# Optimization experiments

Measured on AMD Instinct MI355X. Metric: run time of the kernel, lower is better.

The kernel has to match this reference:

```python
import jax, jax.numpy as jnp
import numpy as np

N, C_IN, C_OUT, T, V = 64, 128, 128, 128, 25
REL = C_IN // 8  # rel_channels = 16


def setup_inputs() -> dict:
    key = jax.random.key(0)
    ks = jax.random.split(key, 12)
    s_in = 1.0 / np.sqrt(C_IN)
    s_rel = 1.0 / np.sqrt(REL)
    return {
        "x": jax.random.normal(ks[0], (N, C_IN, T, V), jnp.float32),
        "A": jax.random.normal(ks[1], (V, V), jnp.float32),
        "alpha": jnp.float32(1.0),
        "W1": jax.random.normal(ks[2], (REL, C_IN), jnp.float32) * s_in,
        "b1": jnp.zeros((REL,), jnp.float32),
        "W2": jax.random.normal(ks[3], (REL, C_IN), jnp.float32) * s_in,
        "b2": jnp.zeros((REL,), jnp.float32),
        "W3": jax.random.normal(ks[4], (C_OUT, C_IN), jnp.float32) * s_in,
        "b3": jnp.zeros((C_OUT,), jnp.float32),
        "W4": jax.random.normal(ks[5], (C_OUT, REL), jnp.float32) * s_rel,
        "b4": jnp.zeros((C_OUT,), jnp.float32),
    }


def reference(x, A, alpha, W1, b1, W2, b2, W3, b3, W4, b4):
    # conv1(x).mean(-2) and conv2(x).mean(-2): 1x1 conv is linear, so mean over
    # T commutes with it -> compute mean first to avoid an (N,REL,T,V) temp.
    xm = x.mean(axis=2)                                        # (N, C, V)
    x1 = jnp.einsum('rc,ncv->nrv', W1, xm) + b1[None, :, None]  # (N, R, V)
    x2 = jnp.einsum('rc,ncv->nrv', W2, xm) + b2[None, :, None]  # (N, R, V)
    x3 = jnp.einsum('oc,nctv->notv', W3, x) + b3[None, :, None, None]  # (N,O,T,V)
    # tanh of broadcasted pairwise difference: (N, R, V, V)
    d = jnp.tanh(x1[:, :, :, None] - x2[:, :, None, :])
    # conv4 (1x1 over channel dim) -> learned per-channel adjacency
    adj = jnp.einsum('or,nrvu->novu', W4, d) + b4[None, :, None, None]
    adj = adj * alpha + A[None, None, :, :]                    # (N, O, V, V)
    return jnp.einsum('ncvu,nctv->nctu', adj, x3)              # (N, O, T, V)
```

## Files before the change

### kernel.cpp

```cpp
#include <hip/hip_runtime.h>


#define NB   64
#define CIN  128
#define COUT 128
#define TT   128
#define VV   25
#define REL  16

#define JT 25
#define KT 4
#define XF_BYTES (JT * KT * 1024)
#define XH_BYTES 51200
#define X3_STRIDE 1040
#define LDS_BYTES (64 * X3_STRIDE)
#define TSTRIDE 416
#define XMP_PLANE (NB * CIN * VV)

typedef __attribute__((ext_vector_type(8))) short bf16x8;
typedef __attribute__((ext_vector_type(4))) float f32x4;

__device__ inline short f2bf(float f) {
    unsigned u = __float_as_uint(f);
    u += 0x7fff + ((u >> 16) & 1);
    return (short)(u >> 16);
}

__launch_bounds__(256)
__global__ void k_prep(const float* __restrict__ x, float* __restrict__ xmp,
                       char* __restrict__ Xf) {
    __shared__ float tile[32 * TSTRIDE];
    int tid = threadIdx.x;
    int kt = blockIdx.x >> 3, tb = blockIdx.x & 7, n = blockIdx.y;
    int c0 = kt * 32;

    const float* src = x + (size_t)(n * CIN + c0) * 3200 + tb * 400;
#pragma unroll
    for (int p = 0; p < 13; ++p) {
        int i = tid + p * 256;
        if (i < 3200) {
            int c = i / 100, q = i - c * 100;
            int sw = ((c >> 3) & 1) << 4;
            *reinterpret_cast<float4*>(&tile[c * TSTRIDE + ((q * 4) ^ sw)]) =
                *reinterpret_cast<const float4*>(src + (size_t)c * 3200 + q * 4);
        }
    }
    __syncthreads();

#pragma unroll
    for (int pp = 0; pp < 4; ++pp) {
        int p = tid + pp * 256;
        if (p < 800) {
            int c = p / 25, v = p - c * 25;
            int sw = ((c >> 3) & 1) << 4;
            float s = 0.f;
#pragma unroll
            for (int t = 0; t < 16; ++t) s += tile[c * TSTRIDE + ((t * 25 + v) ^ sw)];
            xmp[(size_t)tb * XMP_PLANE + ((size_t)n * CIN + c0 + c) * VV + v] = s;
        }
    }

    char* dst = Xf + (size_t)(n * 8 + tb) * XF_BYTES + (size_t)kt * 25600;
    for (int ch = tid; ch < 1600; ch += 256) {
        int l = ch & 63, jt = ch >> 6;
        int j = jt * 16 + (l & 15);
        int cl = 8 * (l >> 4);
        int sw = ((l >> 4) & 1) << 4;
        bf16x8 v;
#pragma unroll
        for (int b = 0; b < 8; ++b)
            v[b] = f2bf(tile[(cl + b) * TSTRIDE + (j ^ sw)]);
        *reinterpret_cast<bf16x8*>(dst + (size_t)ch * 16) = v;
    }
}

__global__ void k_adj(const float* __restrict__ xmp,
                      const float* __restrict__ A, const float* __restrict__ alphap,
                      const float* __restrict__ W1, const float* __restrict__ b1,
                      const float* __restrict__ W2, const float* __restrict__ b2,
                      const float* __restrict__ W4, const float* __restrict__ b4,
                      const float* __restrict__ W3, char* __restrict__ W3f,
                      char* __restrict__ adjT) {
    __shared__ char adjS[32 * 2048];
    __shared__ float xms[CIN * VV];
    __shared__ float W1s[REL * CIN];
    __shared__ float W2s[REL * CIN];
    __shared__ float x1s[REL * VV];
    __shared__ float x2s[REL * VV];
    __shared__ float W4s[32 * REL];
    __shared__ float b4s[32];

    int tid = threadIdx.x;
    int n = blockIdx.x;
    int o0 = blockIdx.y * 32;

    if (n == 0) {
#pragma unroll
        for (int pass = 0; pass < 2; ++pass) {
            int chunk = blockIdx.y * 512 + pass * 256 + tid;
            int l = chunk & 63;
            int frag = chunk >> 6;
            int ct = frag >> 2, kt = frag & 3;
            int c = ct * 16 + (l & 15);
            int kb = kt * 32 + 8 * (l >> 4);
            const float4 f0 = *reinterpret_cast<const float4*>(&W3[(size_t)c * CIN + kb]);
            const float4 f1 = *reinterpret_cast<const float4*>(&W3[(size_t)c * CIN + kb + 4]);
            bf16x8 vv;
            vv[0] = f2bf(f0.x); vv[1] = f2bf(f0.y); vv[2] = f2bf(f0.z); vv[3] = f2bf(f0.w);
            vv[4] = f2bf(f1.x); vv[5] = f2bf(f1.y); vv[6] = f2bf(f1.z); vv[7] = f2bf(f1.w);
            *reinterpret_cast<bf16x8*>(W3f + (size_t)chunk * 16) = vv;
        }
    }

    for (int i = tid; i < 16384; i += 256) reinterpret_cast<float*>(adjS)[i] = 0.f;
    for (int i = tid; i < CIN * VV; i += 256) {
        float s = 0.f;
#pragma unroll
        for (int tb = 0; tb < 8; ++tb)
            s += xmp[(size_t)tb * XMP_PLANE + (size_t)n * CIN * VV + i];
        xms[i] = s * (1.0f / TT);
    }
    for (int i = tid; i < REL * CIN; i += 256) { W1s[i] = W1[i]; W2s[i] = W2[i]; }
    for (int i = tid; i < 32 * REL; i += 256) W4s[i] = W4[o0 * REL + i];
    if (tid < 32) b4s[tid] = b4[o0 + tid];
    __syncthreads();

    for (int task = tid; task < 2 * REL * VV; task += 256) {
        int rv = task % (REL * VV);
        int which = task / (REL * VV);
        int r = rv / VV, v = rv % VV;
        const float* Ws = which ? W2s : W1s;
        float s = 0.f;
#pragma unroll 8
        for (int c = 0; c < CIN; ++c) s = fmaf(Ws[r * CIN + c], xms[c * VV + v], s);
        s += which ? b2[r] : b1[r];
        (which ? x2s : x1s)[rv] = s;
    }
    __syncthreads();

    float alpha = alphap[0];
    for (int p = tid; p < VV * VV; p += 256) {
        int v = p / VV, u = p % VV;
        float d[REL];
#pragma unroll
        for (int r = 0; r < REL; ++r) d[r] = tanhf(x1s[r * VV + v] - x2s[r * VV + u]);
        float Avu = A[v * VV + u];
        int off = (u >> 4) * 1024 + (((u & 15) + 16 * (v >> 3)) * 16) + (v & 7) * 2;
        for (int oo = 0; oo < 32; ++oo) {
            float s = 0.f;
#pragma unroll
            for (int r = 0; r < REL; ++r) s = fmaf(W4s[oo * REL + r], d[r], s);
            float val = alpha * (s + b4s[oo]) + Avu;
            *(short*)(adjS + oo * 2048 + off) = f2bf(val);
        }
    }
    __syncthreads();

    float4* dst = reinterpret_cast<float4*>(adjT + (size_t)(n * COUT + o0) * 2048);
    const float4* src = reinterpret_cast<const float4*>(adjS);
    for (int i = tid; i < 4096; i += 256) dst[i] = src[i];
}

__launch_bounds__(1024)
__global__ void k_main(const char* __restrict__ Xf, const char* __restrict__ W3f,
                       const float* __restrict__ b3, const char* __restrict__ adjT,
                       float* __restrict__ out) {
    __shared__ __align__(16) char lds[LDS_BYTES];

    int tid = threadIdx.x;
    int tb = blockIdx.x, n = blockIdx.y;
    int lane = tid & 63, w = tid >> 6;
    int g = lane >> 4, lr = lane & 15;
    int ct = w >> 1, jh = w & 1;
    int jt0 = jh ? 13 : 0;
    int njt = jh ? 12 : 13;

    const char* xfb = Xf + (size_t)(n * 8 + tb) * XF_BYTES;

    f32x4 acc[13];
#pragma unroll
    for (int u = 0; u < 13; ++u) acc[u] = f32x4{0.f, 0.f, 0.f, 0.f};

#pragma unroll
    for (int h = 0; h < 2; ++h) {
#pragma unroll
        for (int q = 0; q < 4; ++q) {
            int chunk = tid + q * 1024;
            if (chunk < 3200)
                *reinterpret_cast<bf16x8*>(lds + (size_t)chunk * 16) =
                    *reinterpret_cast<const bf16x8*>(
                        xfb + (size_t)h * XH_BYTES + (size_t)chunk * 16);
        }
        __syncthreads();
#pragma unroll
        for (int kk = 0; kk < 2; ++kk) {
            int kt = h * 2 + kk;
            bf16x8 a = *reinterpret_cast<const bf16x8*>(
                W3f + (size_t)((ct * 4 + kt) * 64 + lane) * 16);
#pragma unroll
            for (int u = 0; u < 13; ++u) {
                if (u < njt) {
                    int jt = jt0 + u;
                    bf16x8 bx = *reinterpret_cast<const bf16x8*>(
                        lds + (size_t)((kk * JT + jt) * 64 + lane) * 16);
                    acc[u] = __builtin_amdgcn_mfma_f32_16x16x32_bf16(a, bx, acc[u], 0, 0, 0);
                }
            }
        }
        __syncthreads();
    }

    float bv[4];
#pragma unroll
    for (int r = 0; r < 4; ++r) bv[r] = b3[ct * 16 + 4 * g + r];

    const char* adjTb = adjT + (size_t)(n * COUT) * 2048;
    int t0 = tb * 16;

#pragma unroll
    for (int hh = 0; hh < 2; ++hh) {
        if ((ct >> 2) == hh) {
            int cb = (ct & 3) * 16 + 4 * g;
#pragma unroll
            for (int u = 0; u < 13; ++u) {
                if (u < njt) {
                    int j = (jt0 + u) * 16 + lr;
                    int t = j / 25, v = j - t * 25;
                    int off = (t + 16 * (v >> 3)) * 16 + (v & 7) * 2;
#pragma unroll
                    for (int r = 0; r < 4; ++r)
                        *(short*)(lds + (size_t)(cb + r) * X3_STRIDE + off) =
                            f2bf(acc[u][r] + bv[r]);
                }
            }
        }
#pragma unroll
        for (int z = 0; z < 7; ++z) {
            int idx = tid + z * 1024;
            if (idx < 7168) {
                int c = idx / 112;
                int rem = idx - c * 112;
                int t = rem / 7, qq = rem - t * 7;
                *(short*)(lds + (size_t)c * X3_STRIDE + (t + 48) * 16 + 2 + qq * 2) = 0;
            }
        }
        __syncthreads();

#pragma unroll
        for (int i = 0; i < 4; ++i) {
            int cl = w * 4 + i;
            int c = hh * 64 + cl;
            bf16x8 a = *reinterpret_cast<const bf16x8*>(
                lds + (size_t)cl * X3_STRIDE + lane * 16);
            const bf16x8* bp = reinterpret_cast<const bf16x8*>(adjTb + (size_t)c * 2048);
            bf16x8 b0 = bp[lane];
            bf16x8 b1 = bp[64 + lane];
            f32x4 z = {0.f, 0.f, 0.f, 0.f};
            f32x4 d0 = __builtin_amdgcn_mfma_f32_16x16x32_bf16(a, b0, z, 0, 0, 0);
            f32x4 d1 = __builtin_amdgcn_mfma_f32_16x16x32_bf16(a, b1, z, 0, 0, 0);
            float* ob = out + ((size_t)(n * COUT + c) * TT + t0) * VV;
#pragma unroll
            for (int rr = 0; rr < 4; ++rr) {
                int t = 4 * g + rr;
                ob[(size_t)t * VV + lr] = d0[rr];
                if (lr < 9) ob[(size_t)t * VV + 16 + lr] = d1[rr];
            }
        }
        __syncthreads();
    }
}

extern "C" void kernel_launch(void* const* d_in, const int* in_sizes, int n_in,
                              void* d_out, int out_size, void* d_ws, size_t ws_size,
                              hipStream_t stream) {
    const float* x     = (const float*)d_in[0];
    const float* A     = (const float*)d_in[1];
    const float* alpha = (const float*)d_in[2];
    const float* W1    = (const float*)d_in[3];
    const float* b1    = (const float*)d_in[4];
    const float* W2    = (const float*)d_in[5];
    const float* b2    = (const float*)d_in[6];
    const float* W3    = (const float*)d_in[7];
    const float* b3    = (const float*)d_in[8];
    const float* W4    = (const float*)d_in[9];
    const float* b4    = (const float*)d_in[10];
    float* out = (float*)d_out;

    float* xmp = (float*)d_ws;
    char* adjT = (char*)d_ws + 6553600;
    char* W3f  = (char*)d_ws + 6553600 + 16777216;
    char* Xf   = (char*)d_ws + 6553600 + 16777216 + 32768;

    k_prep<<<dim3(32, NB), 256, 0, stream>>>(x, xmp, Xf);
    k_adj<<<dim3(NB, 4), 256, 0, stream>>>(xmp, A, alpha, W1, b1, W2, b2, W4, b4,
                                           W3, W3f, adjT);
    k_main<<<dim3(TT / 16, NB), 1024, 0, stream>>>(Xf, W3f, b3, adjT, out);
}
```

Measured before the change: 126.4 us.

## Read X fragments directly from global, remap blocks, use packed bf16 convert

In k_main, the X fragment staging through LDS is removed along with its two barriers. The MFMA B operands are now loaded straight from global memory, and the zero-padding writes are hoisted before the epilogue loop so they run only once. The grid becomes 1D with a swizzled block-to-(n, tb) mapping meant to spread batches across XCDs, and launch bounds gain a min-blocks hint. The conversions in k_prep and k_adj switch to the v_cvt_pk_bf16_f32 instruction. The direct global loads could raise memory latency per MFMA, and with the LDS barrier gone the timing of the epilogue LDS writes now depends on the remaining syncs.

Result: slower. 163.1 us (+29.1%).

```diff
diff --git a/kernel.cpp b/kernel.cpp
--- a/kernel.cpp
+++ b/kernel.cpp
@@ -11,7 +11,6 @@
 #define JT 25
 #define KT 4
 #define XF_BYTES (JT * KT * 1024)
-#define XH_BYTES 51200
 #define X3_STRIDE 1040
 #define LDS_BYTES (64 * X3_STRIDE)
 #define TSTRIDE 416
@@ -24,6 +23,12 @@
     unsigned u = __float_as_uint(f);
     u += 0x7fff + ((u >> 16) & 1);
     return (short)(u >> 16);
+}
+
+__device__ inline unsigned cvtpk(float lo, float hi) {
+    unsigned r;
+    asm("v_cvt_pk_bf16_f32 %0, %1, %2" : "=v"(r) : "v"(lo), "v"(hi));
+    return r;
 }
 
 __launch_bounds__(256)
@@ -66,11 +71,13 @@
         int j = jt * 16 + (l & 15);
         int cl = 8 * (l >> 4);
         int sw = ((l >> 4) & 1) << 4;
-        bf16x8 v;
-#pragma unroll
-        for (int b = 0; b < 8; ++b)
-            v[b] = f2bf(tile[(cl + b) * TSTRIDE + (j ^ sw)]);
-        *reinterpret_cast<bf16x8*>(dst + (size_t)ch * 16) = v;
+        float f[8];
+#pragma unroll
+        for (int b = 0; b < 8; ++b) f[b] = tile[(cl + b) * TSTRIDE + (j ^ sw)];
+        uint4 vv;
+        vv.x = cvtpk(f[0], f[1]); vv.y = cvtpk(f[2], f[3]);
+        vv.z = cvtpk(f[4], f[5]); vv.w = cvtpk(f[6], f[7]);
+        *reinterpret_cast<uint4*>(dst + (size_t)ch * 16) = vv;
     }
 }
 
@@ -105,10 +112,10 @@
             int kb = kt * 32 + 8 * (l >> 4);
             const float4 f0 = *reinterpret_cast<const float4*>(&W3[(size_t)c * CIN + kb]);
             const float4 f1 = *reinterpret_cast<const float4*>(&W3[(size_t)c * CIN + kb + 4]);
-            bf16x8 vv;
-            vv[0] = f2bf(f0.x); vv[1] = f2bf(f0.y); vv[2] = f2bf(f0.z); vv[3] = f2bf(f0.w);
-            vv[4] = f2bf(f1.x); vv[5] = f2bf(f1.y); vv[6] = f2bf(f1.z); vv[7] = f2bf(f1.w);
-            *reinterpret_cast<bf16x8*>(W3f + (size_t)chunk * 16) = vv;
+            uint4 vv;
+            vv.x = cvtpk(f0.x, f0.y); vv.y = cvtpk(f0.z, f0.w);
+            vv.z = cvtpk(f1.x, f1.y); vv.w = cvtpk(f1.z, f1.w);
+            *reinterpret_cast<uint4*>(W3f + (size_t)chunk * 16) = vv;
         }
     }
 
@@ -161,14 +168,16 @@
     for (int i = tid; i < 4096; i += 256) dst[i] = src[i];
 }
 
-__launch_bounds__(1024)
+__launch_bounds__(1024, 8)
 __global__ void k_main(const char* __restrict__ Xf, const char* __restrict__ W3f,
                        const float* __restrict__ b3, const char* __restrict__ adjT,
                        float* __restrict__ out) {
     __shared__ __align__(16) char lds[LDS_BYTES];
 
     int tid = threadIdx.x;
-    int tb = blockIdx.x, n = blockIdx.y;
+    int id = blockIdx.x;
+    int q = id >> 3, r8 = id & 7;
+    int n = r8 * 8 + (q >> 3), tb = q & 7;
     int lane = tid & 63, w = tid >> 6;
     int g = lane >> 4, lr = lane & 15;
     int ct = w >> 1, jh = w & 1;
@@ -180,34 +189,30 @@
     f32x4 acc[13];
 #pragma unroll
     for (int u = 0; u < 13; ++u) acc[u] = f32x4{0.f, 0.f, 0.f, 0.f};
-
-#pragma unroll
-    for (int h = 0; h < 2; ++h) {
-#pragma unroll
-        for (int q = 0; q < 4; ++q) {
-            int chunk = tid + q * 1024;
-            if (chunk < 3200)
-                *reinterpret_cast<bf16x8*>(lds + (size_t)chunk * 16) =
-                    *reinterpret_cast<const bf16x8*>(
-                        xfb + (size_t)h * XH_BYTES + (size_t)chunk * 16);
-        }
-        __syncthreads();
-#pragma unroll
-        for (int kk = 0; kk < 2; ++kk) {
-            int kt = h * 2 + kk;
-            bf16x8 a = *reinterpret_cast<const bf16x8*>(
-                W3f + (size_t)((ct * 4 + kt) * 64 + lane) * 16);
-#pragma unroll
-            for (int u = 0; u < 13; ++u) {
-                if (u < njt) {
-                    int jt = jt0 + u;
-                    bf16x8 bx = *reinterpret_cast<const bf16x8*>(
-                        lds + (size_t)((kk * JT + jt) * 64 + lane) * 16);
-                    acc[u] = __builtin_amdgcn_mfma_f32_16x16x32_bf16(a, bx, acc[u], 0, 0, 0);
-                }
+#pragma unroll
+    for (int kt = 0; kt < KT; ++kt) {
+        bf16x8 a = *reinterpret_cast<const bf16x8*>(
+            W3f + (size_t)((ct * 4 + kt) * 64 + lane) * 16);
+#pragma unroll
+        for (int u = 0; u < 13; ++u) {
+            if (u < njt) {
+                int jt = jt0 + u;
+                bf16x8 bx = *reinterpret_cast<const bf16x8*>(
+                    xfb + (size_t)((kt * JT + jt) * 64 + lane) * 16);
+                acc[u] = __builtin_amdgcn_mfma_f32_16x16x32_bf16(a, bx, acc[u], 0, 0, 0);
             }
         }
-        __syncthreads();
+    }
+
+#pragma unroll
+    for (int z = 0; z < 7; ++z) {
+        int idx = tid + z * 1024;
+        if (idx < 7168) {
+            int c = idx / 112;
+            int rem = idx - c * 112;
+            int t = rem / 7, qq = rem - t * 7;
+            *(short*)(lds + (size_t)c * X3_STRIDE + (t + 48) * 16 + 2 + qq * 2) = 0;
+        }
     }
 
     float bv[4];
@@ -232,16 +237,6 @@
                         *(short*)(lds + (size_t)(cb + r) * X3_STRIDE + off) =
                             f2bf(acc[u][r] + bv[r]);
                 }
-            }
-        }
-#pragma unroll
-        for (int z = 0; z < 7; ++z) {
-            int idx = tid + z * 1024;
-            if (idx < 7168) {
-                int c = idx / 112;
-                int rem = idx - c * 112;
-                int t = rem / 7, qq = rem - t * 7;
-                *(short*)(lds + (size_t)c * X3_STRIDE + (t + 48) * 16 + 2 + qq * 2) = 0;
             }
         }
         __syncthreads();
@@ -294,5 +289,5 @@
     k_prep<<<dim3(32, NB), 256, 0, stream>>>(x, xmp, Xf);
     k_adj<<<dim3(NB, 4), 256, 0, stream>>>(xmp, A, alpha, W1, b1, W2, b2, W4, b4,
                                            W3, W3f, adjT);
-    k_main<<<dim3(TT / 16, NB), 1024, 0, stream>>>(Xf, W3f, b3, adjT, out);
-}
+    k_main<<<dim3(512), 1024, 0, stream>>>(Xf, W3f, b3, adjT, out);
+}
```
